# Kernel optimization log

Hardware: AMD Instinct MI355X
Metric: run time of the kernel (lower is better)

## Reference

```python
import jax, jax.numpy as jnp
import numpy as np

R = 3            # num_relations
H = 256          # hid_dim
N0, N1, N2, N3 = 50000, 10000, 4000, 1024   # sampled node counts per hop
FAN = 16         # in-edges per target node
NB_NODES = 100000


def setup_inputs() -> dict:
    keys = iter(jax.random.split(jax.random.key(0), 80))
    def nrm(shape, scale=1.0):
        return jax.random.normal(next(keys), shape, jnp.float32) * scale
    inp = {}
    inp["features"] = nrm((NB_NODES, H))
    inp["n_ids"] = jax.random.randint(next(keys), (R, N0), 0, NB_NODES)
    def edges(n_src, n_dst):
        src = jax.random.randint(next(keys), (R, n_dst * FAN), 0, n_src)
        dst = jnp.tile(jnp.repeat(jnp.arange(n_dst), FAN)[None, :], (R, 1))
        return src, dst
    inp["src1"], inp["dst1"] = edges(N0, N1)
    inp["src2"], inp["dst2"] = edges(N1, N2)
    inp["src3"], inp["dst3"] = edges(N2, N3)
    def tconv_params(p, din, heads, ch):
        hc = heads * ch
        s = 1.0 / np.sqrt(din)
        for nm in ("Wq", "Wk", "Wv", "Ws"):
            inp[p + nm] = nrm((R, din, hc), s)
        for nm in ("bq", "bk", "bv", "bs"):
            inp[p + nm] = jnp.zeros((R, hc), jnp.float32)
        inp[p + "Wb"] = nrm((R, 3 * hc, 1), 1.0 / np.sqrt(3 * hc))
    tconv_params("l1_", H, 2, H // 2)
    tconv_params("l2_", H, 1, H // 2)
    tconv_params("l3_", H // 2, 1, H)
    inp["w_omega"] = nrm((H, H), 1.0 / np.sqrt(H))
    inp["b_omega"] = jnp.zeros((H,), jnp.float32)
    inp["u_omega"] = nrm((H,), 1.0 / np.sqrt(H))
    inp["rl"] = jnp.ones((R, 1), jnp.float32)
    return inp


def _tconv(x, src, dst, n_dst, P, heads, ch):
    """PyG TransformerConv with beta=True (gated skip), concat heads, eval mode."""
    Wq, bq, Wk, bk, Wv, bv, Ws, bs, Wb = P
    x_dst = x[:n_dst]
    q = (x_dst @ Wq + bq).reshape(n_dst, heads, ch)
    k = (x @ Wk + bk).reshape(-1, heads, ch)
    v = (x @ Wv + bv).reshape(-1, heads, ch)
    logit = (q[dst] * k[src]).sum(-1) * (1.0 / np.sqrt(ch))        # [E, heads]
    m = jax.ops.segment_max(logit, dst, num_segments=n_dst)
    p = jnp.exp(logit - m[dst])
    z = jax.ops.segment_sum(p, dst, num_segments=n_dst)
    a = p / z[dst]                                                  # edge softmax
    out = jax.ops.segment_sum(v[src] * a[..., None], dst, num_segments=n_dst)
    out = out.reshape(n_dst, heads * ch)
    x_r = x_dst @ Ws + bs
    g = jax.nn.sigmoid(jnp.concatenate([out, x_r, out - x_r], -1) @ Wb)
    return g * x_r + (1.0 - g) * out


def _rel_forward(feats, n_id, s1, d1, s2, d2, s3, d3, P1, P2, P3):
    x = feats[n_id]                                     # [N0, H]
    x = _tconv(x, s1, d1, N1, P1, 2, H // 2)            # [N1, H]
    x = (x - x.mean(0)) / jnp.sqrt(x.var(0) + 1e-5)     # BatchNorm1d (batch stats, identity affine)
    x = jax.nn.elu(x)
    x = _tconv(x, s2, d2, N2, P2, 1, H // 2)            # [N2, H/2]
    x = _tconv(x, s3, d3, N3, P3, 1, H)                 # [N3, H]
    return x


def _forward(features, n_ids, src1, dst1, src2, dst2, src3, dst3,
             l1_Wq, l1_bq, l1_Wk, l1_bk, l1_Wv, l1_bv, l1_Ws, l1_bs, l1_Wb,
             l2_Wq, l2_bq, l2_Wk, l2_bk, l2_Wv, l2_bv, l2_Ws, l2_bs, l2_Wb,
             l3_Wq, l3_bq, l3_Wk, l3_bk, l3_Wv, l3_bv, l3_Ws, l3_bs, l3_Wb,
             w_omega, b_omega, u_omega, rl):
    P1 = (l1_Wq, l1_bq, l1_Wk, l1_bk, l1_Wv, l1_bv, l1_Ws, l1_bs, l1_Wb)
    P2 = (l2_Wq, l2_bq, l2_Wk, l2_bk, l2_Wv, l2_bv, l2_Ws, l2_bs, l2_Wb)
    P3 = (l3_Wq, l3_bq, l3_Wk, l3_bk, l3_Wv, l3_bv, l3_Ws, l3_bs, l3_Wb)
    per_rel = jax.vmap(_rel_forward, in_axes=(None, 0, 0, 0, 0, 0, 0, 0, 0, 0, 0))
    emb = per_rel(features, n_ids, src1, dst1, src2, dst2, src3, dst3, P1, P2, P3)  # [R, N3, H]
    multi = emb.transpose(1, 0, 2) * rl[None]            # [N3, R, H], RL-threshold scaled
    v = jnp.tanh(multi @ w_omega + b_omega)              # [N3, R, H]
    alphas = jax.nn.softmax(v @ u_omega, axis=1)         # [N3, R]
    return (multi * alphas[..., None]).sum(1)            # [N3, H]


def reference(features, n_ids, src1, dst1, src2, dst2, src3, dst3,
              l1_Wq, l1_bq, l1_Wk, l1_bk, l1_Wv, l1_bv, l1_Ws, l1_bs, l1_Wb,
              l2_Wq, l2_bq, l2_Wk, l2_bk, l2_Wv, l2_bv, l2_Ws, l2_bs, l2_Wb,
              l3_Wq, l3_bq, l3_Wk, l3_bk, l3_Wv, l3_bv, l3_Ws, l3_bs, l3_Wb,
              w_omega, b_omega, u_omega, rl):
    return _forward(features, n_ids, src1, dst1, src2, dst2, src3, dst3,
                    l1_Wq, l1_bq, l1_Wk, l1_bk, l1_Wv, l1_bv, l1_Ws, l1_bs, l1_Wb,
                    l2_Wq, l2_bq, l2_Wk, l2_bk, l2_Wv, l2_bv, l2_Ws, l2_bs, l2_Wb,
                    l3_Wq, l3_bq, l3_Wk, l3_bk, l3_Wv, l3_bv, l3_Ws, l3_bs, l3_Wb,
                    w_omega, b_omega, u_omega, rl)
```

## Files before the change

### kernel.cpp

```cpp
#include <hip/hip_runtime.h>
#include <hip/hip_bf16.h>
#include <math.h>

#define H 256
#define N0 50000
#define N1 10000
#define N2 4000
#define N3 1024
#define FAN 16

typedef __hip_bfloat16 bf16;
typedef __attribute__((ext_vector_type(8))) short short8;
typedef __attribute__((ext_vector_type(4))) short short4v;
typedef __attribute__((ext_vector_type(2))) short short2v;
typedef __attribute__((ext_vector_type(4))) float floatx4;

typedef const __attribute__((address_space(1))) void* gas_ptr;
typedef __attribute__((address_space(3))) void* las_ptr;

__device__ __forceinline__ void load_lds16(const void* g, void* l) {
    __builtin_amdgcn_global_load_lds((gas_ptr)g, (las_ptr)l, 16, 0, 0);
}

__device__ __forceinline__ float2 cvt_bf2(unsigned u) {
    union { unsigned q; float f; } lo, hi;
    lo.q = u << 16; hi.q = u & 0xffff0000u;
    return make_float2(lo.f, hi.f);
}

template<typename OutT, int K>
__global__ __launch_bounds__(512, 4) void gemm_lds(
    const bf16* __restrict__ A, size_t Astr,
    const bf16* __restrict__ Bt,
    const float* __restrict__ b1, const float* __restrict__ b2, int Nh,
    OutT* __restrict__ C, size_t Cstr, int M, int N)
{
    constexpr int KC = K / 32;
    constexpr int CPR = K / 8;
    constexpr int LOG_CPR = (K == 256) ? 5 : 4;
    constexpr int RPI = 64 / CPR;
    constexpr int ISSUES = 16 / RPI;
    __shared__ bf16 A_s[128 * K];

    const int z = blockIdx.z;
    A  += (size_t)z * Astr;
    Bt += (size_t)z * N * K;
    b1 += (size_t)z * Nh;
    b2 += (size_t)z * Nh;
    C  += (size_t)z * Cstr;

    const int lane = threadIdx.x & 63;
    const int w = threadIdx.x >> 6;
    const int rh = w >> 2;
    const int cg = w & 3;
    const int lm = lane & 15;
    const int q = lane >> 4;
    const int mbase = blockIdx.x * 128;
    const int n0 = blockIdx.y * 256;

    {
        const int ch = lane & (CPR - 1);
        const int rsub = lane >> LOG_CPR;
        #pragma unroll
        for (int i = 0; i < ISSUES; i++) {
            int row = w * 16 + i * RPI + rsub;
            int grow = mbase + row; grow = grow < M ? grow : M - 1;
            int gch = ch ^ (row & 7);
            load_lds16(A + (size_t)grow * K + gch * 8,
                       A_s + (size_t)(w * 16 + i * RPI) * K);
        }
    }

    const bf16* bp[4];
    #pragma unroll
    for (int ni = 0; ni < 4; ni++)
        bp[ni] = Bt + (size_t)(n0 + cg * 64 + ni * 16 + lm) * K + q * 8;

    floatx4 acc[4][4];
    #pragma unroll
    for (int i = 0; i < 4; i++)
        #pragma unroll
        for (int j = 0; j < 4; j++)
            acc[i][j] = (floatx4){0.f, 0.f, 0.f, 0.f};

    __syncthreads();

    short8 bn[4];
    #pragma unroll
    for (int ni = 0; ni < 4; ni++) bn[ni] = *(const short8*)(bp[ni]);

    #pragma unroll
    for (int kc = 0; kc < KC; kc++) {
        short8 bc[4];
        #pragma unroll
        for (int ni = 0; ni < 4; ni++) bc[ni] = bn[ni];
        if (kc + 1 < KC) {
            #pragma unroll
            for (int ni = 0; ni < 4; ni++)
                bn[ni] = *(const short8*)(bp[ni] + (kc + 1) * 32);
        }
        short8 af[4];
        #pragma unroll
        for (int mi = 0; mi < 4; mi++) {
            int row = rh * 64 + mi * 16 + lm;
            af[mi] = *(const short8*)(A_s + row * K + (((kc * 4 + q) ^ (lm & 7)) * 8));
        }
        #pragma unroll
        for (int mi = 0; mi < 4; mi++)
            #pragma unroll
            for (int ni = 0; ni < 4; ni++)
                acc[mi][ni] = __builtin_amdgcn_mfma_f32_16x16x32_bf16(
                    af[mi], bc[ni], acc[mi][ni], 0, 0, 0);
    }

    if constexpr (sizeof(OutT) == 2) {
        __syncthreads();
        bf16* stg = A_s + (size_t)w * (16 * 72);
        #pragma unroll
        for (int p = 0; p < 4; p++) {
            #pragma unroll
            for (int ni = 0; ni < 4; ni++) {
                int colg = n0 + cg * 64 + ni * 16 + lm;
                float bias = (colg < Nh) ? b1[colg] : b2[colg - Nh];
                #pragma unroll
                for (int rg = 0; rg < 4; rg++)
                    stg[(q * 4 + rg) * 72 + ni * 16 + lm] = (bf16)(acc[p][ni][rg] + bias);
            }
            #pragma unroll
            for (int it = 0; it < 2; it++) {
                int rl = it * 8 + (lane >> 3);
                int grow = mbase + rh * 64 + p * 16 + rl;
                short8 vv = *(const short8*)(stg + rl * 72 + (lane & 7) * 8);
                if (grow < M)
                    *(short8*)(C + (size_t)grow * N + n0 + cg * 64 + (lane & 7) * 8) = vv;
            }
        }
    } else {
        #pragma unroll
        for (int ni = 0; ni < 4; ni++) {
            int colg = n0 + cg * 64 + ni * 16 + lm;
            float bias = (colg < Nh) ? b1[colg] : b2[colg - Nh];
            #pragma unroll
            for (int mi = 0; mi < 4; mi++) {
                int rb = mbase + rh * 64 + mi * 16 + q * 4;
                #pragma unroll
                for (int rg = 0; rg < 4; rg++) {
                    int rr = rb + rg;
                    if (rr < M) C[(size_t)rr * N + colg] = acc[mi][ni][rg] + bias;
                }
            }
        }
    }
}

__global__ __launch_bounds__(256) void gather_bf16(
    const float* __restrict__ F, const int* __restrict__ n_ids, bf16* __restrict__ out,
    int nrows)
{
    int z = blockIdx.y;
    const int* idx = n_ids + (size_t)z * nrows;
    bf16* o = out + (size_t)z * nrows * H;
    int t = blockIdx.x * 256 + threadIdx.x;
    int row = t >> 6;
    if (row >= nrows) return;
    int c4 = (t & 63) * 4;
    float4 v = *(const float4*)(F + (size_t)idx[row] * H + c4);
    bf16 tmp[4] = {(bf16)v.x, (bf16)v.y, (bf16)v.z, (bf16)v.w};
    *(short4v*)(o + (size_t)row * H + c4) = *(const short4v*)tmp;
}

__global__ void pack_bt3(const float* __restrict__ W1, const float* __restrict__ W2,
                         bf16* __restrict__ Wt, int K, int Nh)
{
    int r = blockIdx.y;
    int nn = blockIdx.x;
    int k = threadIdx.x;
    size_t wstride = (size_t)K * Nh;
    float v = (nn < Nh) ? W1[r * wstride + (size_t)k * Nh + nn]
                        : W2[r * wstride + (size_t)k * Nh + (nn - Nh)];
    Wt[(size_t)r * 2 * wstride + (size_t)nn * K + k] = (bf16)v;
}

template<int CPLH, int HEADS>
__global__ __launch_bounds__(256) void attn_gate(
    const float* __restrict__ qs, size_t qsStr,
    const bf16* __restrict__ kv, size_t kvStr,
    const int* __restrict__ src,
    const float* __restrict__ Wb,
    float* __restrict__ yf, size_t yfStr,
    bf16* __restrict__ yb, size_t ybStr,
    int ndst, float scale)
{
    constexpr int ch = CPLH * 64;
    constexpr int hc = HEADS * ch;
    constexpr int CPL = HEADS * CPLH;
    const int z = blockIdx.y;
    int lane = threadIdx.x & 63;
    int d = blockIdx.x * 4 + (threadIdx.x >> 6);
    if (d >= ndst) return;
    qs += (size_t)z * qsStr;
    kv += (size_t)z * kvStr;
    src += (size_t)z * ndst * FAN;
    Wb += (size_t)z * 3 * hc;

    const float* qp = qs + (size_t)d * (2 * hc);
    float qv[CPL], xv[CPL];
    #pragma unroll
    for (int h = 0; h < HEADS; h++) {
        if constexpr (CPLH == 2) {
            float2 a = *(const float2*)(qp + h * ch + lane * 2);
            float2 b = *(const float2*)(qp + hc + h * ch + lane * 2);
            qv[h * 2] = a.x; qv[h * 2 + 1] = a.y;
            xv[h * 2] = b.x; xv[h * 2 + 1] = b.y;
        } else {
            float4 a = *(const float4*)(qp + h * ch + lane * 4);
            float4 b = *(const float4*)(qp + hc + h * ch + lane * 4);
            qv[h * 4] = a.x; qv[h * 4 + 1] = a.y; qv[h * 4 + 2] = a.z; qv[h * 4 + 3] = a.w;
            xv[h * 4] = b.x; xv[h * 4 + 1] = b.y; xv[h * 4 + 2] = b.z; xv[h * 4 + 3] = b.w;
        }
    }
    const int* sp = src + (size_t)d * FAN;
    int sidx[FAN];
    #pragma unroll
    for (int e = 0; e < FAN; e++) sidx[e] = sp[e];

    float ov[CPL];
    #pragma unroll
    for (int i = 0; i < CPL; i++) ov[i] = 0.f;

    #pragma unroll
    for (int h = 0; h < HEADS; h++) {
        float logit[FAN], mx = -1e30f;
        #pragma unroll
        for (int e = 0; e < FAN; e++) {
            const bf16* kp = kv + (size_t)sidx[e] * (2 * hc) + h * ch + lane * CPLH;
            float dot;
            if constexpr (CPLH == 2) {
                float2 kf = cvt_bf2(*(const unsigned*)kp);
                dot = qv[h * 2] * kf.x + qv[h * 2 + 1] * kf.y;
            } else {
                uint2 u = *(const uint2*)kp;
                float2 k0 = cvt_bf2(u.x), k1 = cvt_bf2(u.y);
                dot = qv[h * 4] * k0.x + qv[h * 4 + 1] * k0.y
                    + qv[h * 4 + 2] * k1.x + qv[h * 4 + 3] * k1.y;
            }
            #pragma unroll
            for (int off = 32; off > 0; off >>= 1) dot += __shfl_xor(dot, off, 64);
            dot *= scale;
            logit[e] = dot;
            mx = fmaxf(mx, dot);
        }
        float zsum = 0.f, p[FAN];
        #pragma unroll
        for (int e = 0; e < FAN; e++) { p[e] = __expf(logit[e] - mx); zsum += p[e]; }
        float inv = 1.f / zsum;
        #pragma unroll
        for (int e = 0; e < FAN; e++) {
            const bf16* vp = kv + (size_t)sidx[e] * (2 * hc) + hc + h * ch + lane * CPLH;
            if constexpr (CPLH == 2) {
                float2 vf = cvt_bf2(*(const unsigned*)vp);
                ov[h * 2] += p[e] * vf.x; ov[h * 2 + 1] += p[e] * vf.y;
            } else {
                uint2 u = *(const uint2*)vp;
                float2 v0 = cvt_bf2(u.x), v1 = cvt_bf2(u.y);
                ov[h * 4] += p[e] * v0.x; ov[h * 4 + 1] += p[e] * v0.y;
                ov[h * 4 + 2] += p[e] * v1.x; ov[h * 4 + 3] += p[e] * v1.y;
            }
        }
        #pragma unroll
        for (int j = 0; j < CPLH; j++) ov[h * CPLH + j] *= inv;
    }

    float s = 0.f;
    #pragma unroll
    for (int h = 0; h < HEADS; h++)
        #pragma unroll
        for (int j = 0; j < CPLH; j++) {
            int c = h * ch + lane * CPLH + j;
            int i = h * CPLH + j;
            s += ov[i] * Wb[c] + xv[i] * Wb[hc + c] + (ov[i] - xv[i]) * Wb[2 * hc + c];
        }
    #pragma unroll
    for (int off = 32; off > 0; off >>= 1) s += __shfl_xor(s, off, 64);
    float g = 1.f / (1.f + __expf(-s));

    float yv[CPL];
    #pragma unroll
    for (int i = 0; i < CPL; i++) yv[i] = g * xv[i] + (1.f - g) * ov[i];

    #pragma unroll
    for (int h = 0; h < HEADS; h++) {
        if (yf) {
            float* op = yf + (size_t)z * yfStr + (size_t)d * hc + h * ch + lane * CPLH;
            if constexpr (CPLH == 2) *(float2*)op = make_float2(yv[h * 2], yv[h * 2 + 1]);
            else *(float4*)op = make_float4(yv[h * 4], yv[h * 4 + 1], yv[h * 4 + 2], yv[h * 4 + 3]);
        }
        if (yb) {
            bf16* op = yb + (size_t)z * ybStr + (size_t)d * hc + h * ch + lane * CPLH;
            bf16 tmp[CPLH];
            #pragma unroll
            for (int j = 0; j < CPLH; j++) tmp[j] = (bf16)yv[h * CPLH + j];
            if constexpr (CPLH == 2) *(short2v*)op = *(const short2v*)tmp;
            else *(short4v*)op = *(const short4v*)tmp;
        }
    }
}

__global__ __launch_bounds__(256) void colstat_partial(
    const bf16* __restrict__ x, size_t xStr, int M,
    float* __restrict__ ps, float* __restrict__ pss)
{
    int z = blockIdx.y;
    const bf16* xp = x + (size_t)z * xStr;
    int f = threadIdx.x;
    int b = blockIdx.x;
    float s = 0.f, ss = 0.f;
    for (int r = b; r < M; r += 64) {
        float v = (float)xp[(size_t)r * H + f];
        s += v; ss += v * v;
    }
    ps[((size_t)z * 64 + b) * H + f] = s;
    pss[((size_t)z * 64 + b) * H + f] = ss;
}

__global__ __launch_bounds__(256) void colfinal_norm_elu(
    const float* __restrict__ ps, const float* __restrict__ pss,
    bf16* __restrict__ x, size_t xStr, int M)
{
    int z = blockIdx.y;
    bf16* xp = x + (size_t)z * xStr;
    int c = threadIdx.x;
    float s = 0.f, ss = 0.f;
    #pragma unroll 8
    for (int b = 0; b < 64; b++) {
        s += ps[((size_t)z * 64 + b) * H + c];
        ss += pss[((size_t)z * 64 + b) * H + c];
    }
    float mu = s / M;
    float istd = rsqrtf(ss / M - mu * mu + 1e-5f);
    for (int r = blockIdx.x; r < M; r += gridDim.x) {
        float t = ((float)xp[(size_t)r * H + c] - mu) * istd;
        xp[(size_t)r * H + c] = (bf16)(t > 0.f ? t : __expf(t) - 1.0f);
    }
}

__global__ __launch_bounds__(256) void semantic_kernel(
    const float* __restrict__ emb,
    const float* __restrict__ Wo, const float* __restrict__ bo,
    const float* __restrict__ uo, const float* __restrict__ rl,
    float* __restrict__ outp)
{
    __shared__ float m_s[3][H];
    __shared__ float red[H];
    __shared__ float score_s[3];
    int n = blockIdx.x, c = threadIdx.x;
    for (int r = 0; r < 3; r++)
        m_s[r][c] = emb[((size_t)r * N3 + n) * H + c] * rl[r];
    __syncthreads();
    for (int r = 0; r < 3; r++) {
        float t = bo[c];
        for (int k2 = 0; k2 < H; k2++) t += m_s[r][k2] * Wo[k2 * H + c];
        red[c] = tanhf(t) * uo[c];
        __syncthreads();
        for (int s = 128; s > 0; s >>= 1) {
            if (c < s) red[c] += red[c + s];
            __syncthreads();
        }
        if (c == 0) score_s[r] = red[0];
        __syncthreads();
    }
    float s0 = score_s[0], s1 = score_s[1], s2 = score_s[2];
    float mx = fmaxf(s0, fmaxf(s1, s2));
    float e0 = __expf(s0 - mx), e1 = __expf(s1 - mx), e2 = __expf(s2 - mx);
    float zi = 1.0f / (e0 + e1 + e2);
    outp[(size_t)n * H + c] = (m_s[0][c] * e0 + m_s[1][c] * e1 + m_s[2][c] * e2) * zi;
}

extern "C" void kernel_launch(void* const* d_in, const int* in_sizes, int n_in,
                              void* d_out, int out_size, void* d_ws, size_t ws_size,
                              hipStream_t stream) {
    const float* features = (const float*)d_in[0];
    const int*   n_ids    = (const int*)d_in[1];
    const int*   src1     = (const int*)d_in[2];
    const int*   src2     = (const int*)d_in[4];
    const int*   src3     = (const int*)d_in[6];
    const float* l1_Wq = (const float*)d_in[8];
    const float* l1_Wk = (const float*)d_in[9];
    const float* l1_Wv = (const float*)d_in[10];
    const float* l1_Ws = (const float*)d_in[11];
    const float* l1_bq = (const float*)d_in[12];
    const float* l1_bk = (const float*)d_in[13];
    const float* l1_bv = (const float*)d_in[14];
    const float* l1_bs = (const float*)d_in[15];
    const float* l1_Wb = (const float*)d_in[16];
    const float* l2_Wq = (const float*)d_in[17];
    const float* l2_Wk = (const float*)d_in[18];
    const float* l2_Wv = (const float*)d_in[19];
    const float* l2_Ws = (const float*)d_in[20];
    const float* l2_bq = (const float*)d_in[21];
    const float* l2_bk = (const float*)d_in[22];
    const float* l2_bv = (const float*)d_in[23];
    const float* l2_bs = (const float*)d_in[24];
    const float* l2_Wb = (const float*)d_in[25];
    const float* l3_Wq = (const float*)d_in[26];
    const float* l3_Wk = (const float*)d_in[27];
    const float* l3_Wv = (const float*)d_in[28];
    const float* l3_Ws = (const float*)d_in[29];
    const float* l3_bq = (const float*)d_in[30];
    const float* l3_bk = (const float*)d_in[31];
    const float* l3_bv = (const float*)d_in[32];
    const float* l3_bs = (const float*)d_in[33];
    const float* l3_Wb = (const float*)d_in[34];
    const float* w_omega = (const float*)d_in[35];
    const float* b_omega = (const float*)d_in[36];
    const float* u_omega = (const float*)d_in[37];
    const float* rl      = (const float*)d_in[38];

    float* ws = (float*)d_ws;
    size_t o = 0;
    float* emb = ws + o; o += (size_t)3 * N3 * H;
    float* qs1 = ws + o; o += (size_t)3 * N1 * 512;
    float* qs2 = ws + o; o += (size_t)3 * N2 * 256;
    float* qs3 = ws + o; o += (size_t)3 * N3 * 512;
    float* ps  = ws + o; o += (size_t)3 * 64 * H;
    float* pss = ws + o; o += (size_t)3 * 64 * H;

    bf16* bws = (bf16*)(ws + o);
    size_t b = 0;
    bf16* Xg  = bws + b; b += (size_t)3 * N0 * H;
    bf16* kv1 = bws + b; b += (size_t)3 * N0 * 512;
    bf16* x1b = bws + b; b += (size_t)3 * N1 * 256;
    bf16* kv2 = bws + b; b += (size_t)3 * N1 * 256;
    bf16* x2b = bws + b; b += (size_t)3 * N2 * 128;
    bf16* kv3 = bws + b; b += (size_t)3 * N2 * 512;
    bf16* Wkv1 = bws + b; b += (size_t)3 * 512 * H;
    bf16* Wqs1 = bws + b; b += (size_t)3 * 512 * H;
    bf16* Wkv2 = bws + b; b += (size_t)3 * 256 * H;
    bf16* Wqs2 = bws + b; b += (size_t)3 * 256 * H;
    bf16* Wkv3 = bws + b; b += (size_t)3 * 512 * 128;
    bf16* Wqs3 = bws + b; b += (size_t)3 * 512 * 128;

    const float sc128 = 0.088388347648318447f;
    const float sc256 = 0.0625f;

    pack_bt3<<<dim3(512, 3), 256, 0, stream>>>(l1_Wk, l1_Wv, Wkv1, 256, 256);
    pack_bt3<<<dim3(512, 3), 256, 0, stream>>>(l1_Wq, l1_Ws, Wqs1, 256, 256);
    pack_bt3<<<dim3(256, 3), 256, 0, stream>>>(l2_Wk, l2_Wv, Wkv2, 256, 128);
    pack_bt3<<<dim3(256, 3), 256, 0, stream>>>(l2_Wq, l2_Ws, Wqs2, 256, 128);
    pack_bt3<<<dim3(512, 3), 128, 0, stream>>>(l3_Wk, l3_Wv, Wkv3, 128, 256);
    pack_bt3<<<dim3(512, 3), 128, 0, stream>>>(l3_Wq, l3_Ws, Wqs3, 128, 256);

    gather_bf16<<<dim3((N0 * 64 + 255) / 256, 3), 256, 0, stream>>>(
        features, n_ids, Xg, N0);

    gemm_lds<bf16, 256><<<dim3((N0 + 127) / 128, 2, 3), 512, 0, stream>>>(
        Xg, (size_t)N0 * H, Wkv1, l1_bk, l1_bv, 256, kv1, (size_t)N0 * 512, N0, 512);
    gemm_lds<float, 256><<<dim3((N1 + 127) / 128, 2, 3), 512, 0, stream>>>(
        Xg, (size_t)N0 * H, Wqs1, l1_bq, l1_bs, 256, qs1, (size_t)N1 * 512, N1, 512);
    attn_gate<2, 2><<<dim3((N1 + 3) / 4, 3), 256, 0, stream>>>(
        qs1, (size_t)N1 * 512, kv1, (size_t)N0 * 512, src1, l1_Wb,
        (float*)nullptr, 0, x1b, (size_t)N1 * 256, N1, sc128);
    colstat_partial<<<dim3(64, 3), 256, 0, stream>>>(x1b, (size_t)N1 * 256, N1, ps, pss);
    colfinal_norm_elu<<<dim3(128, 3), 256, 0, stream>>>(ps, pss, x1b, (size_t)N1 * 256, N1);

    gemm_lds<bf16, 256><<<dim3((N1 + 127) / 128, 1, 3), 512, 0, stream>>>(
        x1b, (size_t)N1 * 256, Wkv2, l2_bk, l2_bv, 128, kv2, (size_t)N1 * 256, N1, 256);
    gemm_lds<float, 256><<<dim3((N2 + 127) / 128, 1, 3), 512, 0, stream>>>(
        x1b, (size_t)N1 * 256, Wqs2, l2_bq, l2_bs, 128, qs2, (size_t)N2 * 256, N2, 256);
    attn_gate<2, 1><<<dim3((N2 + 3) / 4, 3), 256, 0, stream>>>(
        qs2, (size_t)N2 * 256, kv2, (size_t)N1 * 256, src2, l2_Wb,
        (float*)nullptr, 0, x2b, (size_t)N2 * 128, N2, sc128);

    gemm_lds<bf16, 128><<<dim3((N2 + 127) / 128, 2, 3), 512, 0, stream>>>(
        x2b, (size_t)N2 * 128, Wkv3, l3_bk, l3_bv, 256, kv3, (size_t)N2 * 512, N2, 512);
    gemm_lds<float, 128><<<dim3((N3 + 127) / 128, 2, 3), 512, 0, stream>>>(
        x2b, (size_t)N2 * 128, Wqs3, l3_bq, l3_bs, 256, qs3, (size_t)N3 * 512, N3, 512);
    attn_gate<4, 1><<<dim3((N3 + 3) / 4, 3), 256, 0, stream>>>(
        qs3, (size_t)N3 * 512, kv3, (size_t)N2 * 512, src3, l3_Wb,
        emb, (size_t)N3 * H, (bf16*)nullptr, 0, N3, sc256);

    semantic_kernel<<<N3, 256, 0, stream>>>(emb, w_omega, b_omega, u_omega, rl, (float*)d_out);
}
```

Before: 663.4 us.

## Merge KV and QS GEMMs into one launch, shrink tiles, restructure attention lanes

Replaces the separate KV and QS projection GEMM launches per layer with one dual kernel that picks weights, biases and outputs by block index, and shrinks the tile to 64 rows with 256 threads. Merges the six weight-pack launches into a single kernel indexed by job. Rewrites attn_gate so each lane holds contiguous channels across all heads: the per-head dot products are done with partial shuffle reductions over lanes per head, and K and V are loaded once per edge instead of once per head. The aim is less launch overhead, better GPU fill on small layers, and fewer, wider gathers, at the cost of more blocks and more per-block B traffic from the smaller M tile.

```diff
diff --git a/kernel.cpp b/kernel.cpp
--- a/kernel.cpp
+++ b/kernel.cpp
@@ -28,34 +28,38 @@
     return make_float2(lo.f, hi.f);
 }
 
-template<typename OutT, int K>
-__global__ __launch_bounds__(512, 4) void gemm_lds(
+template<int K>
+__global__ __launch_bounds__(256, 4) void gemm_dual(
     const bf16* __restrict__ A, size_t Astr,
-    const bf16* __restrict__ Bt,
-    const float* __restrict__ b1, const float* __restrict__ b2, int Nh,
-    OutT* __restrict__ C, size_t Cstr, int M, int N)
+    const bf16* __restrict__ BtKV, const bf16* __restrict__ BtQS,
+    const float* __restrict__ bk, const float* __restrict__ bv,
+    const float* __restrict__ bq, const float* __restrict__ bs, int Nh,
+    bf16* __restrict__ Ckv, size_t CkvStr, int Mkv,
+    float* __restrict__ Cqs, size_t CqsStr, int Mqs,
+    int nbKV)
 {
     constexpr int KC = K / 32;
     constexpr int CPR = K / 8;
     constexpr int LOG_CPR = (K == 256) ? 5 : 4;
     constexpr int RPI = 64 / CPR;
     constexpr int ISSUES = 16 / RPI;
-    __shared__ bf16 A_s[128 * K];
+    const int N = 2 * Nh;
+    __shared__ bf16 A_s[64 * K];
 
     const int z = blockIdx.z;
-    A  += (size_t)z * Astr;
-    Bt += (size_t)z * N * K;
-    b1 += (size_t)z * Nh;
-    b2 += (size_t)z * Nh;
-    C  += (size_t)z * Cstr;
+    const bool isKV = (int)blockIdx.x < nbKV;
+    const int bx = isKV ? blockIdx.x : blockIdx.x - nbKV;
+    const int M = isKV ? Mkv : Mqs;
+    const bf16* Bt = (isKV ? BtKV : BtQS) + (size_t)z * N * K;
+    const float* b1 = (isKV ? bk : bq) + (size_t)z * Nh;
+    const float* b2 = (isKV ? bv : bs) + (size_t)z * Nh;
+    A += (size_t)z * Astr;
 
     const int lane = threadIdx.x & 63;
     const int w = threadIdx.x >> 6;
-    const int rh = w >> 2;
-    const int cg = w & 3;
     const int lm = lane & 15;
     const int q = lane >> 4;
-    const int mbase = blockIdx.x * 128;
+    const int mbase = bx * 64;
     const int n0 = blockIdx.y * 256;
 
     {
@@ -74,7 +78,7 @@
     const bf16* bp[4];
     #pragma unroll
     for (int ni = 0; ni < 4; ni++)
-        bp[ni] = Bt + (size_t)(n0 + cg * 64 + ni * 16 + lm) * K + q * 8;
+        bp[ni] = Bt + (size_t)(n0 + w * 64 + ni * 16 + lm) * K + q * 8;
 
     floatx4 acc[4][4];
     #pragma unroll
@@ -102,7 +106,7 @@
         short8 af[4];
         #pragma unroll
         for (int mi = 0; mi < 4; mi++) {
-            int row = rh * 64 + mi * 16 + lm;
+            int row = mi * 16 + lm;
             af[mi] = *(const short8*)(A_s + row * K + (((kc * 4 + q) ^ (lm & 7)) * 8));
         }
         #pragma unroll
@@ -113,14 +117,15 @@
                     af[mi], bc[ni], acc[mi][ni], 0, 0, 0);
     }
 
-    if constexpr (sizeof(OutT) == 2) {
+    if (isKV) {
+        bf16* C = Ckv + (size_t)z * CkvStr;
         __syncthreads();
         bf16* stg = A_s + (size_t)w * (16 * 72);
         #pragma unroll
         for (int p = 0; p < 4; p++) {
             #pragma unroll
             for (int ni = 0; ni < 4; ni++) {
-                int colg = n0 + cg * 64 + ni * 16 + lm;
+                int colg = n0 + w * 64 + ni * 16 + lm;
                 float bias = (colg < Nh) ? b1[colg] : b2[colg - Nh];
                 #pragma unroll
                 for (int rg = 0; rg < 4; rg++)
@@ -129,20 +134,21 @@
             #pragma unroll
             for (int it = 0; it < 2; it++) {
                 int rl = it * 8 + (lane >> 3);
-                int grow = mbase + rh * 64 + p * 16 + rl;
+                int grow = mbase + p * 16 + rl;
                 short8 vv = *(const short8*)(stg + rl * 72 + (lane & 7) * 8);
                 if (grow < M)
-                    *(short8*)(C + (size_t)grow * N + n0 + cg * 64 + (lane & 7) * 8) = vv;
+                    *(short8*)(C + (size_t)grow * N + n0 + w * 64 + (lane & 7) * 8) = vv;
             }
         }
     } else {
+        float* C = Cqs + (size_t)z * CqsStr;
         #pragma unroll
         for (int ni = 0; ni < 4; ni++) {
-            int colg = n0 + cg * 64 + ni * 16 + lm;
+            int colg = n0 + w * 64 + ni * 16 + lm;
             float bias = (colg < Nh) ? b1[colg] : b2[colg - Nh];
             #pragma unroll
             for (int mi = 0; mi < 4; mi++) {
-                int rb = mbase + rh * 64 + mi * 16 + q * 4;
+                int rb = mbase + mi * 16 + q * 4;
                 #pragma unroll
                 for (int rg = 0; rg < 4; rg++) {
                     int rr = rb + rg;
@@ -169,19 +175,35 @@
     *(short4v*)(o + (size_t)row * H + c4) = *(const short4v*)tmp;
 }
 
-__global__ void pack_bt3(const float* __restrict__ W1, const float* __restrict__ W2,
-                         bf16* __restrict__ Wt, int K, int Nh)
-{
-    int r = blockIdx.y;
-    int nn = blockIdx.x;
-    int k = threadIdx.x;
+__global__ __launch_bounds__(256) void pack_all(
+    const float* __restrict__ l1_Wk, const float* __restrict__ l1_Wv,
+    const float* __restrict__ l1_Wq, const float* __restrict__ l1_Ws,
+    const float* __restrict__ l2_Wk, const float* __restrict__ l2_Wv,
+    const float* __restrict__ l2_Wq, const float* __restrict__ l2_Ws,
+    const float* __restrict__ l3_Wk, const float* __restrict__ l3_Wv,
+    const float* __restrict__ l3_Wq, const float* __restrict__ l3_Ws,
+    bf16* __restrict__ Wkv1, bf16* __restrict__ Wqs1,
+    bf16* __restrict__ Wkv2, bf16* __restrict__ Wqs2,
+    bf16* __restrict__ Wkv3, bf16* __restrict__ Wqs3)
+{
+    int job = blockIdx.z, r = blockIdx.y, nn = blockIdx.x, k = threadIdx.x;
+    const float *W1, *W2; bf16* Wt; int K, Nh;
+    switch (job) {
+        case 0: W1 = l1_Wk; W2 = l1_Wv; Wt = Wkv1; K = 256; Nh = 256; break;
+        case 1: W1 = l1_Wq; W2 = l1_Ws; Wt = Wqs1; K = 256; Nh = 256; break;
+        case 2: W1 = l2_Wk; W2 = l2_Wv; Wt = Wkv2; K = 256; Nh = 128; break;
+        case 3: W1 = l2_Wq; W2 = l2_Ws; Wt = Wqs2; K = 256; Nh = 128; break;
+        case 4: W1 = l3_Wk; W2 = l3_Wv; Wt = Wkv3; K = 128; Nh = 256; break;
+        default: W1 = l3_Wq; W2 = l3_Ws; Wt = Wqs3; K = 128; Nh = 256; break;
+    }
+    if (nn >= 2 * Nh || k >= K) return;
     size_t wstride = (size_t)K * Nh;
-    float v = (nn < Nh) ? W1[r * wstride + (size_t)k * Nh + nn]
-                        : W2[r * wstride + (size_t)k * Nh + (nn - Nh)];
+    float v = (nn < Nh) ? W1[(size_t)r * wstride + (size_t)k * Nh + nn]
+                        : W2[(size_t)r * wstride + (size_t)k * Nh + (nn - Nh)];
     Wt[(size_t)r * 2 * wstride + (size_t)nn * K + k] = (bf16)v;
 }
 
-template<int CPLH, int HEADS>
+template<int CPL, int HEADS>
 __global__ __launch_bounds__(256) void attn_gate(
     const float* __restrict__ qs, size_t qsStr,
     const bf16* __restrict__ kv, size_t kvStr,
@@ -191,9 +213,8 @@
     bf16* __restrict__ yb, size_t ybStr,
     int ndst, float scale)
 {
-    constexpr int ch = CPLH * 64;
-    constexpr int hc = HEADS * ch;
-    constexpr int CPL = HEADS * CPLH;
+    constexpr int hc = CPL * 64;
+    constexpr int LPH = 64 / HEADS;
     const int z = blockIdx.y;
     int lane = threadIdx.x & 63;
     int d = blockIdx.x * 4 + (threadIdx.x >> 6);
@@ -203,106 +224,96 @@
     src += (size_t)z * ndst * FAN;
     Wb += (size_t)z * 3 * hc;
 
-    const float* qp = qs + (size_t)d * (2 * hc);
+    const float* qp = qs + (size_t)d * (2 * hc) + lane * CPL;
     float qv[CPL], xv[CPL];
-    #pragma unroll
-    for (int h = 0; h < HEADS; h++) {
-        if constexpr (CPLH == 2) {
-            float2 a = *(const float2*)(qp + h * ch + lane * 2);
-            float2 b = *(const float2*)(qp + hc + h * ch + lane * 2);
-            qv[h * 2] = a.x; qv[h * 2 + 1] = a.y;
-            xv[h * 2] = b.x; xv[h * 2 + 1] = b.y;
-        } else {
-            float4 a = *(const float4*)(qp + h * ch + lane * 4);
-            float4 b = *(const float4*)(qp + hc + h * ch + lane * 4);
-            qv[h * 4] = a.x; qv[h * 4 + 1] = a.y; qv[h * 4 + 2] = a.z; qv[h * 4 + 3] = a.w;
-            xv[h * 4] = b.x; xv[h * 4 + 1] = b.y; xv[h * 4 + 2] = b.z; xv[h * 4 + 3] = b.w;
-        }
+    if constexpr (CPL == 2) {
+        float2 a = *(const float2*)qp;
+        float2 b = *(const float2*)(qp + hc);
+        qv[0] = a.x; qv[1] = a.y; xv[0] = b.x; xv[1] = b.y;
+    } else {
+        float4 a = *(const float4*)qp;
+        float4 b = *(const float4*)(qp + hc);
+        qv[0] = a.x; qv[1] = a.y; qv[2] = a.z; qv[3] = a.w;
+        xv[0] = b.x; xv[1] = b.y; xv[2] = b.z; xv[3] = b.w;
     }
     const int* sp = src + (size_t)d * FAN;
     int sidx[FAN];
     #pragma unroll
     for (int e = 0; e < FAN; e++) sidx[e] = sp[e];
 
+    float part[FAN];
+    #pragma unroll
+    for (int e = 0; e < FAN; e++) {
+        const bf16* kp = kv + (size_t)sidx[e] * (2 * hc) + lane * CPL;
+        if constexpr (CPL == 2) {
+            float2 kf = cvt_bf2(*(const unsigned*)kp);
+            part[e] = qv[0] * kf.x + qv[1] * kf.y;
+        } else {
+            uint2 u = *(const uint2*)kp;
+            float2 k0 = cvt_bf2(u.x), k1 = cvt_bf2(u.y);
+            part[e] = qv[0] * k0.x + qv[1] * k0.y + qv[2] * k1.x + qv[3] * k1.y;
+        }
+    }
+    float logit[FAN], mx = -1e30f;
+    #pragma unroll
+    for (int e = 0; e < FAN; e++) {
+        float dt = part[e];
+        #pragma unroll
+        for (int off = LPH / 2; off > 0; off >>= 1) dt += __shfl_xor(dt, off, 64);
+        dt *= scale;
+        logit[e] = dt;
+        mx = fmaxf(mx, dt);
+    }
+    float zsum = 0.f, p[FAN];
+    #pragma unroll
+    for (int e = 0; e < FAN; e++) { p[e] = __expf(logit[e] - mx); zsum += p[e]; }
+    float inv = 1.f / zsum;
+
     float ov[CPL];
     #pragma unroll
-    for (int i = 0; i < CPL; i++) ov[i] = 0.f;
-
-    #pragma unroll
-    for (int h = 0; h < HEADS; h++) {
-        float logit[FAN], mx = -1e30f;
-        #pragma unroll
-        for (int e = 0; e < FAN; e++) {
-            const bf16* kp = kv + (size_t)sidx[e] * (2 * hc) + h * ch + lane * CPLH;
-            float dot;
-            if constexpr (CPLH == 2) {
-                float2 kf = cvt_bf2(*(const unsigned*)kp);
-                dot = qv[h * 2] * kf.x + qv[h * 2 + 1] * kf.y;
-            } else {
-                uint2 u = *(const uint2*)kp;
-                float2 k0 = cvt_bf2(u.x), k1 = cvt_bf2(u.y);
-                dot = qv[h * 4] * k0.x + qv[h * 4 + 1] * k0.y
-                    + qv[h * 4 + 2] * k1.x + qv[h * 4 + 3] * k1.y;
-            }
-            #pragma unroll
-            for (int off = 32; off > 0; off >>= 1) dot += __shfl_xor(dot, off, 64);
-            dot *= scale;
-            logit[e] = dot;
-            mx = fmaxf(mx, dot);
-        }
-        float zsum = 0.f, p[FAN];
-        #pragma unroll
-        for (int e = 0; e < FAN; e++) { p[e] = __expf(logit[e] - mx); zsum += p[e]; }
-        float inv = 1.f / zsum;
-        #pragma unroll
-        for (int e = 0; e < FAN; e++) {
-            const bf16* vp = kv + (size_t)sidx[e] * (2 * hc) + hc + h * ch + lane * CPLH;
-            if constexpr (CPLH == 2) {
-                float2 vf = cvt_bf2(*(const unsigned*)vp);
-                ov[h * 2] += p[e] * vf.x; ov[h * 2 + 1] += p[e] * vf.y;
-            } else {
-                uint2 u = *(const uint2*)vp;
-                float2 v0 = cvt_bf2(u.x), v1 = cvt_bf2(u.y);
-                ov[h * 4] += p[e] * v0.x; ov[h * 4 + 1] += p[e] * v0.y;
-                ov[h * 4 + 2] += p[e] * v1.x; ov[h * 4 + 3] += p[e] * v1.y;
-            }
-        }
-        #pragma unroll
-        for (int j = 0; j < CPLH; j++) ov[h * CPLH + j] *= inv;
-    }
+    for (int j = 0; j < CPL; j++) ov[j] = 0.f;
+    #pragma unroll
+    for (int e = 0; e < FAN; e++) {
+        const bf16* vp = kv + (size_t)sidx[e] * (2 * hc) + hc + lane * CPL;
+        if constexpr (CPL == 2) {
+            float2 vf = cvt_bf2(*(const unsigned*)vp);
+            ov[0] += p[e] * vf.x; ov[1] += p[e] * vf.y;
+        } else {
+            uint2 u = *(const uint2*)vp;
+            float2 v0 = cvt_bf2(u.x), v1 = cvt_bf2(u.y);
+            ov[0] += p[e] * v0.x; ov[1] += p[e] * v0.y;
+            ov[2] += p[e] * v1.x; ov[3] += p[e] * v1.y;
+        }
+    }
+    #pragma unroll
+    for (int j = 0; j < CPL; j++) ov[j] *= inv;
 
     float s = 0.f;
     #pragma unroll
-    for (int h = 0; h < HEADS; h++)
-        #pragma unroll
-        for (int j = 0; j < CPLH; j++) {
-            int c = h * ch + lane * CPLH + j;
-            int i = h * CPLH + j;
-            s += ov[i] * Wb[c] + xv[i] * Wb[hc + c] + (ov[i] - xv[i]) * Wb[2 * hc + c];
-        }
+    for (int j = 0; j < CPL; j++) {
+        int c = lane * CPL + j;
+        s += ov[j] * Wb[c] + xv[j] * Wb[hc + c] + (ov[j] - xv[j]) * Wb[2 * hc + c];
+    }
     #pragma unroll
     for (int off = 32; off > 0; off >>= 1) s += __shfl_xor(s, off, 64);
     float g = 1.f / (1.f + __expf(-s));
 
     float yv[CPL];
     #pragma unroll
-    for (int i = 0; i < CPL; i++) yv[i] = g * xv[i] + (1.f - g) * ov[i];
-
-    #pragma unroll
-    for (int h = 0; h < HEADS; h++) {
-        if (yf) {
-            float* op = yf + (size_t)z * yfStr + (size_t)d * hc + h * ch + lane * CPLH;
-            if constexpr (CPLH == 2) *(float2*)op = make_float2(yv[h * 2], yv[h * 2 + 1]);
-            else *(float4*)op = make_float4(yv[h * 4], yv[h * 4 + 1], yv[h * 4 + 2], yv[h * 4 + 3]);
-        }
-        if (yb) {
-            bf16* op = yb + (size_t)z * ybStr + (size_t)d * hc + h * ch + lane * CPLH;
-            bf16 tmp[CPLH];
-            #pragma unroll
-            for (int j = 0; j < CPLH; j++) tmp[j] = (bf16)yv[h * CPLH + j];
-            if constexpr (CPLH == 2) *(short2v*)op = *(const short2v*)tmp;
-            else *(short4v*)op = *(const short4v*)tmp;
-        }
+    for (int j = 0; j < CPL; j++) yv[j] = g * xv[j] + (1.f - g) * ov[j];
+
+    if (yf) {
+        float* op = yf + (size_t)z * yfStr + (size_t)d * hc + lane * CPL;
+        if constexpr (CPL == 2) *(float2*)op = make_float2(yv[0], yv[1]);
+        else *(float4*)op = make_float4(yv[0], yv[1], yv[2], yv[3]);
+    }
+    if (yb) {
+        bf16* op = yb + (size_t)z * ybStr + (size_t)d * hc + lane * CPL;
+        bf16 tmp[CPL];
+        #pragma unroll
+        for (int j = 0; j < CPL; j++) tmp[j] = (bf16)yv[j];
+        if constexpr (CPL == 2) *(short2v*)op = *(const short2v*)tmp;
+        else *(short4v*)op = *(const short4v*)tmp;
     }
 }
 
@@ -443,38 +454,41 @@
     const float sc128 = 0.088388347648318447f;
     const float sc256 = 0.0625f;
 
-    pack_bt3<<<dim3(512, 3), 256, 0, stream>>>(l1_Wk, l1_Wv, Wkv1, 256, 256);
-    pack_bt3<<<dim3(512, 3), 256, 0, stream>>>(l1_Wq, l1_Ws, Wqs1, 256, 256);
-    pack_bt3<<<dim3(256, 3), 256, 0, stream>>>(l2_Wk, l2_Wv, Wkv2, 256, 128);
-    pack_bt3<<<dim3(256, 3), 256, 0, stream>>>(l2_Wq, l2_Ws, Wqs2, 256, 128);
-    pack_bt3<<<dim3(512, 3), 128, 0, stream>>>(l3_Wk, l3_Wv, Wkv3, 128, 256);
-    pack_bt3<<<dim3(512, 3), 128, 0, stream>>>(l3_Wq, l3_Ws, Wqs3, 128, 256);
+    pack_all<<<dim3(512, 3, 6), 256, 0, stream>>>(
+        l1_Wk, l1_Wv, l1_Wq, l1_Ws, l2_Wk, l2_Wv, l2_Wq, l2_Ws,
+        l3_Wk, l3_Wv, l3_Wq, l3_Ws, Wkv1, Wqs1, Wkv2, Wqs2, Wkv3, Wqs3);
 
     gather_bf16<<<dim3((N0 * 64 + 255) / 256, 3), 256, 0, stream>>>(
         features, n_ids, Xg, N0);
 
-    gemm_lds<bf16, 256><<<dim3((N0 + 127) / 128, 2, 3), 512, 0, stream>>>(
-        Xg, (size_t)N0 * H, Wkv1, l1_bk, l1_bv, 256, kv1, (size_t)N0 * 512, N0, 512);
-    gemm_lds<float, 256><<<dim3((N1 + 127) / 128, 2, 3), 512, 0, stream>>>(
-        Xg, (size_t)N0 * H, Wqs1, l1_bq, l1_bs, 256, qs1, (size_t)N1 * 512, N1, 512);
-    attn_gate<2, 2><<<dim3((N1 + 3) / 4, 3), 256, 0, stream>>>(
+    {
+        int nbKV = (N0 + 63) / 64, nbQS = (N1 + 63) / 64;
+        gemm_dual<256><<<dim3(nbKV + nbQS, 2, 3), 256, 0, stream>>>(
+            Xg, (size_t)N0 * H, Wkv1, Wqs1, l1_bk, l1_bv, l1_bq, l1_bs, 256,
+            kv1, (size_t)N0 * 512, N0, qs1, (size_t)N1 * 512, N1, nbKV);
+    }
+    attn_gate<4, 2><<<dim3((N1 + 3) / 4, 3), 256, 0, stream>>>(
         qs1, (size_t)N1 * 512, kv1, (size_t)N0 * 512, src1, l1_Wb,
         (float*)nullptr, 0, x1b, (size_t)N1 * 256, N1, sc128);
     colstat_partial<<<dim3(64, 3), 256, 0, stream>>>(x1b, (size_t)N1 * 256, N1, ps, pss);
     colfinal_norm_elu<<<dim3(128, 3), 256, 0, stream>>>(ps, pss, x1b, (size_t)N1 * 256, N1);
 
-    gemm_lds<bf16, 256><<<dim3((N1 + 127) / 128, 1, 3), 512, 0, stream>>>(
-        x1b, (size_t)N1 * 256, Wkv2, l2_bk, l2_bv, 128, kv2, (size_t)N1 * 256, N1, 256);
-    gemm_lds<float, 256><<<dim3((N2 + 127) / 128, 1, 3), 512, 0, stream>>>(
-        x1b, (size_t)N1 * 256, Wqs2, l2_bq, l2_bs, 128, qs2, (size_t)N2 * 256, N2, 256);
+    {
+        int nbKV = (N1 + 63) / 64, nbQS = (N2 + 63) / 64;
+        gemm_dual<256><<<dim3(nbKV + nbQS, 1, 3), 256, 0, stream>>>(
+            x1b, (size_t)N1 * 256, Wkv2, Wqs2, l2_bk, l2_bv, l2_bq, l2_bs, 128,
+            kv2, (size_t)N1 * 256, N1, qs2, (size_t)N2 * 256, N2, nbKV);
+    }
     attn_gate<2, 1><<<dim3((N2 + 3) / 4, 3), 256, 0, stream>>>(
         qs2, (size_t)N2 * 256, kv2, (size_t)N1 * 256, src2, l2_Wb,
         (float*)nullptr, 0, x2b, (size_t)N2 * 128, N2, sc128);
 
-    gemm_lds<bf16, 128><<<dim3((N2 + 127) / 128, 2, 3), 512, 0, stream>>>(
-        x2b, (size_t)N2 * 128, Wkv3, l3_bk, l3_bv, 256, kv3, (size_t)N2 * 512, N2, 512);
-    gemm_lds<float, 128><<<dim3((N3 + 127) / 128, 2, 3), 512, 0, stream>>>(
-        x2b, (size_t)N2 * 128, Wqs3, l3_bq, l3_bs, 256, qs3, (size_t)N3 * 512, N3, 512);
+    {
+        int nbKV = (N2 + 63) / 64, nbQS = (N3 + 63) / 64;
+        gemm_dual<128><<<dim3(nbKV + nbQS, 2, 3), 256, 0, stream>>>(
+            x2b, (size_t)N2 * 128, Wkv3, Wqs3, l3_bk, l3_bv, l3_bq, l3_bs, 256,
+            kv3, (size_t)N2 * 512, N2, qs3, (size_t)N3 * 512, N3, nbKV);
+    }
     attn_gate<4, 1><<<dim3((N3 + 3) / 4, 3), 256, 0, stream>>>(
         qs3, (size_t)N3 * 512, kv3, (size_t)N2 * 512, src3, l3_Wb,
         emb, (size_t)N3 * H, (bf16*)nullptr, 0, N3, sc256);
```

Result: faster. 612.7 us (-7.6%).
